# Performance work log

Measured on AMD Instinct MI355X. Metric: run time of the kernel, lower is better.

## Reference

```python
import jax, jax.numpy as jnp
import numpy as np

N = 100000          # nodes
E = 1000000         # edges (before self-loops)
NFEAT = 512
NHID = 32
HEADS = 8
NCLASS = 40
SLOPE = 0.2         # PyG GATConv negative_slope


def gat_conv(x, W, a_src, a_dst, bias, src, dst, heads, out_c, concat):
    """PyG-style GATConv (eval mode, self-loops already appended to src/dst)."""
    n = x.shape[0]
    h = (x @ W).reshape(n, heads, out_c)                      # [N, H, C]
    e_src = jnp.sum(h * a_src, axis=-1)                       # [N, H]
    e_dst = jnp.sum(h * a_dst, axis=-1)                       # [N, H]
    e = jax.nn.leaky_relu(e_src[src] + e_dst[dst], SLOPE)     # [E, H]
    m = jax.ops.segment_max(e, dst, num_segments=n)           # per-dst max
    ex = jnp.exp(e - m[dst])
    den = jax.ops.segment_sum(ex, dst, num_segments=n)        # [N, H]
    alpha = ex / den[dst]                                     # softmax over in-edges
    out = jax.ops.segment_sum(alpha[:, :, None] * h[src], dst, num_segments=n)
    out = out.reshape(n, heads * out_c) if concat else out.mean(axis=1)
    return out + bias


def setup_inputs() -> dict:
    key = jax.random.key(0)
    ks = jax.random.split(key, 10)
    x = jax.random.normal(ks[0], (N, NFEAT), dtype=jnp.float32)
    edge_index = jax.random.randint(ks[1], (2, E), 0, N, dtype=jnp.int64)
    s1 = 1.0 / np.sqrt(NFEAT)
    s2 = 1.0 / np.sqrt(HEADS * NHID)
    return {
        "x": x,
        "edge_index": edge_index,
        "W1": jax.random.normal(ks[2], (NFEAT, HEADS * NHID), dtype=jnp.float32) * s1,
        "a_src1": jax.random.normal(ks[3], (HEADS, NHID), dtype=jnp.float32) * s2,
        "a_dst1": jax.random.normal(ks[4], (HEADS, NHID), dtype=jnp.float32) * s2,
        "b1": jnp.zeros((HEADS * NHID,), dtype=jnp.float32),
        "W2": jax.random.normal(ks[5], (HEADS * NHID, NCLASS), dtype=jnp.float32) * s2,
        "a_src2": jax.random.normal(ks[6], (1, NCLASS), dtype=jnp.float32) * 0.1,
        "a_dst2": jax.random.normal(ks[7], (1, NCLASS), dtype=jnp.float32) * 0.1,
        "b2": jnp.zeros((NCLASS,), dtype=jnp.float32),
    }


def reference(x, edge_index, W1, a_src1, a_dst1, b1, W2, a_src2, a_dst2, b2):
    loop = jnp.arange(N, dtype=edge_index.dtype)
    src = jnp.concatenate([edge_index[0], loop])
    dst = jnp.concatenate([edge_index[1], loop])
    # layer 1: nfeat -> heads*nhid (concat), ELU  (dropout is identity in eval)
    h1 = jax.nn.elu(gat_conv(x, W1, a_src1, a_dst1, b1, src, dst, HEADS, NHID, True))
    # layer 2: heads*nhid -> nclass, single head, concat=False
    logits = gat_conv(h1, W2, a_src2, a_dst2, b2, src, dst, 1, NCLASS, False)
    return jax.nn.log_softmax(logits, axis=1), h1
```

## Files before the change

kernel.cpp:

```cpp
#include <hip/hip_runtime.h>

#define NN 100000
#define EE 1000000
#define NFEAT 512
#define NHID 32
#define HEADS 8
#define F1 256
#define NCLASS 40
#define SLOPE 0.2f
#define NB1 98

typedef __bf16 bf16x8 __attribute__((ext_vector_type(8)));
typedef float f32x4 __attribute__((ext_vector_type(4)));

union BF8 { unsigned short s[8]; bf16x8 v; uint4 u; };

__device__ __forceinline__ float bf2f(unsigned short u) {
    return __uint_as_float(((unsigned)u) << 16);
}
__device__ __forceinline__ unsigned short f2bf(float f) {
    unsigned x = __float_as_uint(f);
    unsigned r = (x + 0x7fffu + ((x >> 16) & 1u)) >> 16;
    return (unsigned short)r;
}
__device__ __forceinline__ float lrelu(float x) { return x > 0.f ? x : SLOPE * x; }

__global__ void detect_i64(const int* __restrict__ ei, int* __restrict__ flag) {
    int i = blockIdx.x * 256 + threadIdx.x;
    if (i < 4096) {
        if (ei[2 * i + 1] != 0) atomicOr(flag, 1);
    }
}
__global__ void canon_edges(const int* __restrict__ ei, const int* __restrict__ flag,
                            int* __restrict__ srcC, int* __restrict__ dstC) {
    int e = blockIdx.x * 256 + threadIdx.x;
    if (e >= EE) return;
    if (*flag) {
        srcC[e] = ei[e];
        dstC[e] = ei[EE + e];
    } else {
        srcC[e] = ei[2 * e];
        dstC[e] = ei[2 * EE + 2 * e];
    }
}

__global__ void count_deg(const int* __restrict__ dstC, int* __restrict__ deg) {
    int e = blockIdx.x * 256 + threadIdx.x;
    if (e < EE) atomicAdd(deg + dstC[e], 1);
}
__global__ void scan1(const int* __restrict__ deg, int* __restrict__ bsum) {
    __shared__ int s[256];
    int b = blockIdx.x, t = threadIdx.x;
    int base = b * 1024 + t * 4, sum = 0;
    #pragma unroll
    for (int j = 0; j < 4; j++) { int i = base + j; sum += (i < NN) ? deg[i] : 0; }
    s[t] = sum; __syncthreads();
    for (int off = 128; off > 0; off >>= 1) {
        if (t < off) s[t] += s[t + off];
        __syncthreads();
    }
    if (t == 0) bsum[b] = s[0];
}
__global__ void scan2(int* __restrict__ bsum, int* __restrict__ row_ptr) {
    if (threadIdx.x == 0 && blockIdx.x == 0) {
        int acc = 0;
        for (int i = 0; i < NB1; i++) { int v = bsum[i]; bsum[i] = acc; acc += v; }
        row_ptr[NN] = EE;
    }
}
__global__ void scan3(const int* __restrict__ deg, const int* __restrict__ bsum,
                      int* __restrict__ row_ptr, int* __restrict__ pos) {
    __shared__ int ts[256];
    int b = blockIdx.x, t = threadIdx.x;
    int base = b * 1024 + t * 4;
    int v[4], sum = 0;
    #pragma unroll
    for (int j = 0; j < 4; j++) { int i = base + j; v[j] = (i < NN) ? deg[i] : 0; sum += v[j]; }
    ts[t] = sum; __syncthreads();
    for (int off = 1; off < 256; off <<= 1) {
        int add = (t >= off) ? ts[t - off] : 0;
        __syncthreads();
        ts[t] += add;
        __syncthreads();
    }
    int prefix = bsum[b] + ts[t] - sum;
    #pragma unroll
    for (int j = 0; j < 4; j++) {
        int i = base + j;
        if (i < NN) { row_ptr[i] = prefix; pos[i] = prefix; prefix += v[j]; }
    }
}
__global__ void fill_csr(const int* __restrict__ srcC, const int* __restrict__ dstC,
                         int* __restrict__ pos, int* __restrict__ eadj) {
    int e = blockIdx.x * 256 + threadIdx.x;
    if (e >= EE) return;
    int idx = atomicAdd(pos + dstC[e], 1);
    eadj[idx] = srcC[e];
}

__global__ void prep_w1(const float* __restrict__ w1, unsigned short* __restrict__ w1tb) {
    int t = blockIdx.x * 256 + threadIdx.x;
    if (t < NFEAT * F1) {
        int k = t / F1, n = t % F1;
        w1tb[n * NFEAT + k] = f2bf(w1[t]);
    }
}

__device__ __forceinline__ void stage_b(const unsigned short* __restrict__ w1tb,
                                        unsigned short* bs, int kk, int tid) {
    #pragma unroll
    for (int j = 0; j < 4; j++) {
        int c = j * 256 + tid;
        int n = c >> 2, part = c & 3;
        const unsigned short* src = w1tb + n * NFEAT + kk * 32 + part * 8;
        unsigned short* dst = bs + c * 8;
        __builtin_amdgcn_global_load_lds(
            (const __attribute__((address_space(1))) unsigned int*)src,
            (__attribute__((address_space(3))) unsigned int*)dst, 16, 0, 0);
    }
}

__global__ __launch_bounds__(256) void gemm1_kernel(
    const float* __restrict__ x, const unsigned short* __restrict__ w1tb,
    unsigned short* __restrict__ hb) {
    __shared__ unsigned short Bs[2][256 * 32];
    int tid = threadIdx.x;
    int wave = tid >> 6, lane = tid & 63;
    int quad = lane >> 4, r = lane & 15;
    int mBase = blockIdx.x * 64 + wave * 16;
    long arow = mBase + r; if (arow > NN - 1) arow = NN - 1;
    const float* aptr = x + arow * NFEAT + quad * 8;

    stage_b(w1tb, Bs[0], 0, tid);

    f32x4 acc[16];
    #pragma unroll
    for (int t = 0; t < 16; t++) acc[t] = {0.f, 0.f, 0.f, 0.f};

    for (int kk = 0; kk < 16; kk++) {
        float4 fa0 = *(const float4*)(aptr + kk * 32);
        float4 fa1 = *(const float4*)(aptr + kk * 32 + 4);
        float fa[8] = {fa0.x, fa0.y, fa0.z, fa0.w, fa1.x, fa1.y, fa1.z, fa1.w};
        BF8 ah;
        #pragma unroll
        for (int j = 0; j < 8; j++) ah.s[j] = f2bf(fa[j]);
        __syncthreads();
        if (kk + 1 < 16) stage_b(w1tb, Bs[(kk + 1) & 1], kk + 1, tid);
        const unsigned short* bsc = Bs[kk & 1];
        #pragma unroll
        for (int t = 0; t < 16; t++) {
            BF8 vb;
            vb.u = *(const uint4*)(bsc + (t * 16 + r) * 32 + quad * 8);
            acc[t] = __builtin_amdgcn_mfma_f32_16x16x32_bf16(ah.v, vb.v, acc[t], 0, 0, 0);
        }
    }
    #pragma unroll
    for (int i = 0; i < 4; i++) {
        int m = mBase + quad * 4 + i;
        if (m < NN) {
            unsigned short* hp = hb + (long)m * F1 + r;
            #pragma unroll
            for (int t = 0; t < 16; t++) hp[t * 16] = f2bf(acc[t][i]);
        }
    }
}

__global__ __launch_bounds__(256) void escore1_kernel(
    const unsigned short* __restrict__ hb, const float* __restrict__ a_src,
    const float* __restrict__ a_dst, float* __restrict__ es, float* __restrict__ ed) {
    __shared__ float As[F1], Ad[F1];
    int tid = threadIdx.x;
    As[tid] = a_src[tid];
    Ad[tid] = a_dst[tid];
    __syncthreads();
    int t = blockIdx.x * 256 + tid;
    if (t >= NN * HEADS) return;
    int n = t >> 3, hd = t & 7;
    const uint4* hp = (const uint4*)(hb + (long)n * F1 + hd * NHID);
    float s = 0.f, d = 0.f;
    #pragma unroll
    for (int q = 0; q < 4; q++) {
        uint4 u = hp[q];
        unsigned vv[4] = {u.x, u.y, u.z, u.w};
        #pragma unroll
        for (int w = 0; w < 4; w++) {
            float lo = bf2f((unsigned short)(vv[w] & 0xffffu));
            float hi = bf2f((unsigned short)(vv[w] >> 16));
            int c = q * 8 + w * 2;
            s += lo * As[hd * NHID + c] + hi * As[hd * NHID + c + 1];
            d += lo * Ad[hd * NHID + c] + hi * Ad[hd * NHID + c + 1];
        }
    }
    es[t] = s; ed[t] = d;
}

__global__ __launch_bounds__(256) void gat1_fused(
    const int* __restrict__ row_ptr, const int* __restrict__ eadj,
    const float* __restrict__ es, const float* __restrict__ ed,
    const unsigned short* __restrict__ hb, const float* __restrict__ b1,
    float* __restrict__ h1o) {
    int wave = threadIdx.x >> 6, lane = threadIdx.x & 63;
    int d = blockIdx.x * 4 + wave;
    if (d >= NN) return;
    int eslot = lane >> 3, hd8 = lane & 7, hdo = lane >> 3;
    float edv = ed[d * 8 + hd8];
    int beg = row_ptr[d], end = row_ptr[d + 1];

    float mself = lrelu(es[d * 8 + hd8] + edv);
    float m = mself;
    for (int i = beg; i < end; i += 8) {
        int idx = i + eslot;
        int s = (idx < end) ? eadj[idx] : 0;
        float el = lrelu(es[s * 8 + hd8] + edv);
        if (idx >= end) el = -1e30f;
        m = fmaxf(m, el);
    }
    m = fmaxf(m, __shfl_xor(m, 8));
    m = fmaxf(m, __shfl_xor(m, 16));
    m = fmaxf(m, __shfl_xor(m, 32));

    float wself = __expf(mself - m);
    float den = (eslot == 0) ? wself : 0.f;
    float wselfo = __shfl(wself, hdo);
    ushort4 hv = ((const ushort4*)(hb + (long)d * F1))[lane];
    float ax = wselfo * bf2f(hv.x), ay = wselfo * bf2f(hv.y);
    float az = wselfo * bf2f(hv.z), aw = wselfo * bf2f(hv.w);

    for (int i = beg; i < end; i += 8) {
        int idx = i + eslot;
        int s = (idx < end) ? eadj[idx] : 0;
        float el = lrelu(es[s * 8 + hd8] + edv);
        float wj = (idx < end) ? __expf(el - m) : 0.f;
        den += wj;
        int cnt = min(8, end - i);
        if (cnt == 8) {
            #pragma unroll
            for (int j = 0; j < 8; j++) {
                float w = __shfl(wj, j * 8 + hdo);
                int sj = __shfl(s, j * 8);
                ushort4 v = ((const ushort4*)(hb + (long)sj * F1))[lane];
                ax += w * bf2f(v.x); ay += w * bf2f(v.y);
                az += w * bf2f(v.z); aw += w * bf2f(v.w);
            }
        } else {
            for (int j = 0; j < cnt; j++) {
                float w = __shfl(wj, j * 8 + hdo);
                int sj = __shfl(s, j * 8);
                ushort4 v = ((const ushort4*)(hb + (long)sj * F1))[lane];
                ax += w * bf2f(v.x); ay += w * bf2f(v.y);
                az += w * bf2f(v.z); aw += w * bf2f(v.w);
            }
        }
    }
    den += __shfl_xor(den, 8);
    den += __shfl_xor(den, 16);
    den += __shfl_xor(den, 32);
    float deno = __shfl(den, hdo);

    float4 bb = ((const float4*)b1)[lane];
    float inv = 1.f / deno;
    float rx = ax * inv + bb.x, ry = ay * inv + bb.y;
    float rz = az * inv + bb.z, rw = aw * inv + bb.w;
    rx = rx > 0.f ? rx : expm1f(rx);
    ry = ry > 0.f ? ry : expm1f(ry);
    rz = rz > 0.f ? rz : expm1f(rz);
    rw = rw > 0.f ? rw : expm1f(rw);
    float4 r = {rx, ry, rz, rw};
    ((float4*)(h1o + (long)d * F1))[lane] = r;
}

__global__ __launch_bounds__(256) void gemm2_kernel(const float* __restrict__ h1,
                                                    const float* __restrict__ w2,
                                                    float* __restrict__ h2) {
    __shared__ float4 Ws[F1 * 10];
    for (int i = threadIdx.x; i < F1 * 10; i += 256) Ws[i] = ((const float4*)w2)[i];
    __syncthreads();
    long t = (long)blockIdx.x * 256 + threadIdx.x;
    if (t >= (long)NN * 10) return;
    int n = (int)(t / 10);
    int j = (int)(t - (long)n * 10);
    const float4* hp = (const float4*)(h1 + (long)n * F1);
    float4 a = {0.f, 0.f, 0.f, 0.f};
    #pragma unroll 8
    for (int k4 = 0; k4 < 64; k4++) {
        float4 hv = hp[k4];
        float4 w0 = Ws[(k4 * 4 + 0) * 10 + j];
        float4 w1v = Ws[(k4 * 4 + 1) * 10 + j];
        float4 w2v = Ws[(k4 * 4 + 2) * 10 + j];
        float4 w3v = Ws[(k4 * 4 + 3) * 10 + j];
        a.x += hv.x * w0.x + hv.y * w1v.x + hv.z * w2v.x + hv.w * w3v.x;
        a.y += hv.x * w0.y + hv.y * w1v.y + hv.z * w2v.y + hv.w * w3v.y;
        a.z += hv.x * w0.z + hv.y * w1v.z + hv.z * w2v.z + hv.w * w3v.z;
        a.w += hv.x * w0.w + hv.y * w1v.w + hv.z * w2v.w + hv.w * w3v.w;
    }
    ((float4*)(h2 + (long)n * NCLASS))[j] = a;
}

__global__ void escore2_kernel(const float* __restrict__ h2,
                               const float* __restrict__ a_src2,
                               const float* __restrict__ a_dst2,
                               float* __restrict__ e2s, float* __restrict__ e2d) {
    __shared__ float As[NCLASS], Ad[NCLASS];
    if (threadIdx.x < NCLASS) {
        As[threadIdx.x] = a_src2[threadIdx.x];
        Ad[threadIdx.x] = a_dst2[threadIdx.x];
    }
    __syncthreads();
    int n = blockIdx.x * 256 + threadIdx.x;
    if (n >= NN) return;
    const float* hp = h2 + (long)n * NCLASS;
    float s = 0.f, d = 0.f;
    #pragma unroll
    for (int c = 0; c < NCLASS; c++) {
        float v = hp[c];
        s += v * As[c];
        d += v * Ad[c];
    }
    e2s[n] = s; e2d[n] = d;
}

__global__ __launch_bounds__(256) void gat2_logsm(
    const int* __restrict__ row_ptr, const int* __restrict__ eadj,
    const float* __restrict__ e2s, const float* __restrict__ e2d,
    const float* __restrict__ h2, const float* __restrict__ b2,
    float* __restrict__ out0) {
    int wave = threadIdx.x >> 6, lane = threadIdx.x & 63;
    int d = blockIdx.x * 4 + wave;
    if (d >= NN) return;
    float edv = e2d[d];
    int beg = row_ptr[d], end = row_ptr[d + 1];

    float mself = lrelu(e2s[d] + edv);
    float m = mself;
    for (int i = beg; i < end; i += 64) {
        int idx = i + lane;
        int s = (idx < end) ? eadj[idx] : 0;
        float el = lrelu(e2s[s] + edv);
        if (idx >= end) el = -1e30f;
        m = fmaxf(m, el);
    }
    #pragma unroll
    for (int off = 32; off; off >>= 1) m = fmaxf(m, __shfl_xor(m, off));

    float den = __expf(mself - m);
    float acc = (lane < NCLASS) ? den * h2[(long)d * NCLASS + lane] : 0.f;
    for (int i = beg; i < end; i += 64) {
        int idx = i + lane;
        int s = (idx < end) ? eadj[idx] : 0;
        float el = lrelu(e2s[s] + edv);
        float wj = (idx < end) ? __expf(el - m) : 0.f;
        int cnt = min(64, end - i);
        for (int j = 0; j < cnt; j++) {
            float w = __shfl(wj, j);
            int sj = __shfl(s, j);
            if (lane < NCLASS) acc += w * h2[(long)sj * NCLASS + lane];
        }
        den += wj;
    }
    float dpart = den;
    #pragma unroll
    for (int off = 32; off; off >>= 1) dpart += __shfl_xor(dpart, off);
    float dfull = dpart - 63.f * __expf(mself - m);

    float v = (lane < NCLASS) ? acc / dfull + b2[lane] : -1e30f;
    float mx = v;
    #pragma unroll
    for (int off = 32; off; off >>= 1) mx = fmaxf(mx, __shfl_xor(mx, off));
    float ex = (lane < NCLASS) ? __expf(v - mx) : 0.f;
    float sm = ex;
    #pragma unroll
    for (int off = 32; off; off >>= 1) sm += __shfl_xor(sm, off);
    float ls = mx + logf(sm);
    if (lane < NCLASS) out0[(long)d * NCLASS + lane] = v - ls;
}

extern "C" void kernel_launch(void* const* d_in, const int* in_sizes, int n_in,
                              void* d_out, int out_size, void* d_ws, size_t ws_size,
                              hipStream_t stream) {
    const float* x   = (const float*)d_in[0];
    const int* ei    = (const int*)d_in[1];
    const float* W1  = (const float*)d_in[2];
    const float* as1 = (const float*)d_in[3];
    const float* ad1 = (const float*)d_in[4];
    const float* b1  = (const float*)d_in[5];
    const float* W2  = (const float*)d_in[6];
    const float* as2 = (const float*)d_in[7];
    const float* ad2 = (const float*)d_in[8];
    const float* b2  = (const float*)d_in[9];

    float* out0 = (float*)d_out;
    float* h1o  = out0 + (long)NN * NCLASS;

    unsigned short* hb = (unsigned short*)d_ws;
    unsigned short* w1tb = hb + (long)NN * F1;
    float* es1  = (float*)(w1tb + F1 * NFEAT);
    float* ed1  = es1 + NN * HEADS;
    float* e2s  = ed1 + NN * HEADS;
    float* e2d  = e2s + NN;
    int* srcC   = (int*)(e2d + NN);
    int* dstC   = srcC + EE;
    int* eadj   = dstC + EE;
    int* deg    = eadj + EE;
    int* row_ptr= deg + NN;
    int* pos    = row_ptr + NN + 1;
    int* bsum   = pos + NN;
    int* flag   = bsum + NB1;
    float* h2   = (float*)d_ws;

    hipMemsetAsync(flag, 0, 4, stream);
    hipMemsetAsync(deg, 0, (size_t)NN * 4, stream);

    detect_i64<<<16, 256, 0, stream>>>(ei, flag);
    canon_edges<<<(EE + 255) / 256, 256, 0, stream>>>(ei, flag, srcC, dstC);
    count_deg<<<(EE + 255) / 256, 256, 0, stream>>>(dstC, deg);
    scan1<<<NB1, 256, 0, stream>>>(deg, bsum);
    scan2<<<1, 64, 0, stream>>>(bsum, row_ptr);
    scan3<<<NB1, 256, 0, stream>>>(deg, bsum, row_ptr, pos);
    fill_csr<<<(EE + 255) / 256, 256, 0, stream>>>(srcC, dstC, pos, eadj);

    prep_w1<<<(NFEAT * F1 + 255) / 256, 256, 0, stream>>>(W1, w1tb);
    gemm1_kernel<<<(NN + 63) / 64, 256, 0, stream>>>(x, w1tb, hb);
    escore1_kernel<<<(NN * HEADS) / 256, 256, 0, stream>>>(hb, as1, ad1, es1, ed1);
    gat1_fused<<<(NN + 3) / 4, 256, 0, stream>>>(row_ptr, eadj, es1, ed1, hb, b1, h1o);

    gemm2_kernel<<<(int)(((long)NN * 10 + 255) / 256), 256, 0, stream>>>(h1o, W2, h2);
    escore2_kernel<<<(NN + 255) / 256, 256, 0, stream>>>(h2, as2, ad2, e2s, e2d);
    gat2_logsm<<<(NN + 3) / 4, 256, 0, stream>>>(row_ptr, eadj, e2s, e2d, h2, b2, out0);
}
```

Baseline: 766.4 us.

## Use online softmax in GAT aggregations, restructure layer-2 lanes, fuse degree count

Degree counting is folded into the edge canonicalization kernel, which removes one launch and a re-read of dst. Both GAT aggregation kernels switch to an online softmax with a running max and rescaling, so each node's edge list is read once instead of twice. Layer 2 is remapped so that 8 edges are processed in parallel, each by 8 lanes holding 5 classes, replacing serial per-edge shuffles. The trade-off is extra exp and rescale work per 8-edge chunk and cross-lane reductions at the end.

```diff
diff --git a/kernel.cpp b/kernel.cpp
--- a/kernel.cpp
+++ b/kernel.cpp
@@ -32,22 +32,23 @@
     }
 }
 __global__ void canon_edges(const int* __restrict__ ei, const int* __restrict__ flag,
-                            int* __restrict__ srcC, int* __restrict__ dstC) {
+                            int* __restrict__ srcC, int* __restrict__ dstC,
+                            int* __restrict__ deg) {
     int e = blockIdx.x * 256 + threadIdx.x;
     if (e >= EE) return;
+    int s, d;
     if (*flag) {
-        srcC[e] = ei[e];
-        dstC[e] = ei[EE + e];
+        s = ei[e];
+        d = ei[EE + e];
     } else {
-        srcC[e] = ei[2 * e];
-        dstC[e] = ei[2 * EE + 2 * e];
-    }
-}
-
-__global__ void count_deg(const int* __restrict__ dstC, int* __restrict__ deg) {
-    int e = blockIdx.x * 256 + threadIdx.x;
-    if (e < EE) atomicAdd(deg + dstC[e], 1);
-}
+        s = ei[2 * e];
+        d = ei[2 * EE + 2 * e];
+    }
+    srcC[e] = s;
+    dstC[e] = d;
+    atomicAdd(deg + d, 1);
+}
+
 __global__ void scan1(const int* __restrict__ deg, int* __restrict__ bsum) {
     __shared__ int s[256];
     int b = blockIdx.x, t = threadIdx.x;
@@ -208,28 +209,27 @@
 
     float mself = lrelu(es[d * 8 + hd8] + edv);
     float m = mself;
+    float den = (eslot == 0) ? 1.f : 0.f;
+    ushort4 hv = ((const ushort4*)(hb + (long)d * F1))[lane];
+    float ax = bf2f(hv.x), ay = bf2f(hv.y);
+    float az = bf2f(hv.z), aw = bf2f(hv.w);
+
     for (int i = beg; i < end; i += 8) {
         int idx = i + eslot;
         int s = (idx < end) ? eadj[idx] : 0;
         float el = lrelu(es[s * 8 + hd8] + edv);
         if (idx >= end) el = -1e30f;
-        m = fmaxf(m, el);
-    }
-    m = fmaxf(m, __shfl_xor(m, 8));
-    m = fmaxf(m, __shfl_xor(m, 16));
-    m = fmaxf(m, __shfl_xor(m, 32));
-
-    float wself = __expf(mself - m);
-    float den = (eslot == 0) ? wself : 0.f;
-    float wselfo = __shfl(wself, hdo);
-    ushort4 hv = ((const ushort4*)(hb + (long)d * F1))[lane];
-    float ax = wselfo * bf2f(hv.x), ay = wselfo * bf2f(hv.y);
-    float az = wselfo * bf2f(hv.z), aw = wselfo * bf2f(hv.w);
-
-    for (int i = beg; i < end; i += 8) {
-        int idx = i + eslot;
-        int s = (idx < end) ? eadj[idx] : 0;
-        float el = lrelu(es[s * 8 + hd8] + edv);
+        float gm = el;
+        gm = fmaxf(gm, __shfl_xor(gm, 8));
+        gm = fmaxf(gm, __shfl_xor(gm, 16));
+        gm = fmaxf(gm, __shfl_xor(gm, 32));
+        float mn = fmaxf(m, gm);
+        float rsc = __expf(m - mn);
+        m = mn;
+        den *= rsc;
+        float ro = __shfl(rsc, hdo);
+        ax *= ro; ay *= ro; az *= ro; aw *= ro;
+
         float wj = (idx < end) ? __expf(el - m) : 0.f;
         den += wj;
         int cnt = min(8, end - i);
@@ -327,51 +327,70 @@
     int wave = threadIdx.x >> 6, lane = threadIdx.x & 63;
     int d = blockIdx.x * 4 + wave;
     if (d >= NN) return;
+    int eslot = lane >> 3, c8 = lane & 7;
     float edv = e2d[d];
     int beg = row_ptr[d], end = row_ptr[d + 1];
 
     float mself = lrelu(e2s[d] + edv);
     float m = mself;
-    for (int i = beg; i < end; i += 64) {
-        int idx = i + lane;
+    float den = (eslot == 0) ? 1.f : 0.f;
+    float acc[5];
+    {
+        const float* hp = h2 + (long)d * NCLASS + c8 * 5;
+        #pragma unroll
+        for (int k = 0; k < 5; k++) acc[k] = (eslot == 0) ? hp[k] : 0.f;
+    }
+
+    for (int i = beg; i < end; i += 8) {
+        int idx = i + eslot;
         int s = (idx < end) ? eadj[idx] : 0;
         float el = lrelu(e2s[s] + edv);
         if (idx >= end) el = -1e30f;
-        m = fmaxf(m, el);
-    }
-    #pragma unroll
-    for (int off = 32; off; off >>= 1) m = fmaxf(m, __shfl_xor(m, off));
-
-    float den = __expf(mself - m);
-    float acc = (lane < NCLASS) ? den * h2[(long)d * NCLASS + lane] : 0.f;
-    for (int i = beg; i < end; i += 64) {
-        int idx = i + lane;
-        int s = (idx < end) ? eadj[idx] : 0;
-        float el = lrelu(e2s[s] + edv);
+        float gm = el;
+        gm = fmaxf(gm, __shfl_xor(gm, 8));
+        gm = fmaxf(gm, __shfl_xor(gm, 16));
+        gm = fmaxf(gm, __shfl_xor(gm, 32));
+        float mn = fmaxf(m, gm);
+        float rsc = __expf(m - mn);
+        m = mn;
+        den *= rsc;
+        #pragma unroll
+        for (int k = 0; k < 5; k++) acc[k] *= rsc;
         float wj = (idx < end) ? __expf(el - m) : 0.f;
-        int cnt = min(64, end - i);
-        for (int j = 0; j < cnt; j++) {
-            float w = __shfl(wj, j);
-            int sj = __shfl(s, j);
-            if (lane < NCLASS) acc += w * h2[(long)sj * NCLASS + lane];
+        den += wj;
+        if (idx < end) {
+            const float* hp = h2 + (long)s * NCLASS + c8 * 5;
+            #pragma unroll
+            for (int k = 0; k < 5; k++) acc[k] += wj * hp[k];
         }
-        den += wj;
-    }
-    float dpart = den;
-    #pragma unroll
-    for (int off = 32; off; off >>= 1) dpart += __shfl_xor(dpart, off);
-    float dfull = dpart - 63.f * __expf(mself - m);
-
-    float v = (lane < NCLASS) ? acc / dfull + b2[lane] : -1e30f;
-    float mx = v;
-    #pragma unroll
-    for (int off = 32; off; off >>= 1) mx = fmaxf(mx, __shfl_xor(mx, off));
-    float ex = (lane < NCLASS) ? __expf(v - mx) : 0.f;
-    float sm = ex;
-    #pragma unroll
-    for (int off = 32; off; off >>= 1) sm += __shfl_xor(sm, off);
+    }
+    #pragma unroll
+    for (int off = 8; off <= 32; off <<= 1) {
+        den += __shfl_xor(den, off);
+        #pragma unroll
+        for (int k = 0; k < 5; k++) acc[k] += __shfl_xor(acc[k], off);
+    }
+    float inv = 1.f / den;
+    float v[5];
+    float mx = -1e30f;
+    #pragma unroll
+    for (int k = 0; k < 5; k++) {
+        v[k] = acc[k] * inv + b2[c8 * 5 + k];
+        mx = fmaxf(mx, v[k]);
+    }
+    #pragma unroll
+    for (int off = 1; off <= 4; off <<= 1) mx = fmaxf(mx, __shfl_xor(mx, off));
+    float sm = 0.f;
+    #pragma unroll
+    for (int k = 0; k < 5; k++) sm += __expf(v[k] - mx);
+    #pragma unroll
+    for (int off = 1; off <= 4; off <<= 1) sm += __shfl_xor(sm, off);
     float ls = mx + logf(sm);
-    if (lane < NCLASS) out0[(long)d * NCLASS + lane] = v - ls;
+    if (eslot == 0) {
+        float* op = out0 + (long)d * NCLASS + c8 * 5;
+        #pragma unroll
+        for (int k = 0; k < 5; k++) op[k] = v[k] - ls;
+    }
 }
 
 extern "C" void kernel_launch(void* const* d_in, const int* in_sizes, int n_in,
@@ -411,8 +430,7 @@
     hipMemsetAsync(deg, 0, (size_t)NN * 4, stream);
 
     detect_i64<<<16, 256, 0, stream>>>(ei, flag);
-    canon_edges<<<(EE + 255) / 256, 256, 0, stream>>>(ei, flag, srcC, dstC);
-    count_deg<<<(EE + 255) / 256, 256, 0, stream>>>(dstC, deg);
+    canon_edges<<<(EE + 255) / 256, 256, 0, stream>>>(ei, flag, srcC, dstC, deg);
     scan1<<<NB1, 256, 0, stream>>>(deg, bsum);
     scan2<<<1, 64, 0, stream>>>(bsum, row_ptr);
     scan3<<<NB1, 256, 0, stream>>>(deg, bsum, row_ptr, pos);
```

Result: faster. 716.4 us (-6.5%).
